# Optimization experiments

Measured on AMD Instinct MI355X. Metric: run time of the kernel, lower is better.

## Reference

```python
import jax, jax.numpy as jnp
import numpy as np

# dims: dim=1024, head_dim=64 (fla default) -> 16 heads; lora dims per TMix.__init__
B, T, D = 8, 2048, 1024
H, HD = 16, 64
DECAY_LR, A_LR, V_LR, G_LR = 64, 64, 32, 160
CHUNK = 64  # chunked scan, mirrors 'chunk' mode state passing
LOG_W_SCALE = -0.6065306597126334  # -exp(-0.5), fla rwkv7 decay soft clamp
GN_EPS = HD * 1e-5  # fla: GroupNorm eps = head_dim * norm_eps


def setup_inputs() -> dict:
    key = jax.random.key(0)
    ks = jax.random.split(key, 22)
    rn = lambda k, shape, s=1.0: jax.random.normal(k, shape, jnp.float32) * s
    s_d = 1.0 / np.sqrt(D).astype(np.float32)
    return dict(
        x=rn(ks[0], (B, T, D)),
        v_first=rn(ks[1], (B, T, D)),
        x_x=rn(ks[2], (6, D), 0.1),           # token-shift mix coefficients (r,w,k,v,a,g)
        W_r=rn(ks[3], (D, D), s_d), W_k=rn(ks[4], (D, D), s_d),
        W_v=rn(ks[5], (D, D), s_d), W_o=rn(ks[6], (D, D), s_d),
        w1=rn(ks[7], (D, DECAY_LR), s_d), w2=rn(ks[8], (DECAY_LR, D), 1.0 / np.sqrt(DECAY_LR)), w0=rn(ks[9], (D,), 0.5),
        a1=rn(ks[10], (D, A_LR), s_d), a2=rn(ks[11], (A_LR, D), 1.0 / np.sqrt(A_LR)), a0=rn(ks[12], (D,), 0.5),
        v1=rn(ks[13], (D, V_LR), s_d), v2=rn(ks[14], (V_LR, D), 1.0 / np.sqrt(V_LR)), v0=rn(ks[15], (D,), 0.5),
        g1=rn(ks[16], (D, G_LR), s_d), g2=rn(ks[17], (G_LR, D), 1.0 / np.sqrt(G_LR)),
        k_k=rn(ks[18], (D,), 0.5), k_a=rn(ks[19], (D,), 0.5), r_k=rn(ks[20], (H, HD), 0.5),
        gn_w=jnp.ones((D,), jnp.float32), gn_b=jnp.zeros((D,), jnp.float32),
    )


def _rwkv7_core(r, logw, k, v, a, b):
    # all [B,T,H,HD]; generalized delta rule: S_t = S_{t-1}*exp(w_t) + (S_{t-1} a_t) b_t^T + v_t k_t^T; o_t = S_t r_t
    nC = T // CHUNK
    to_chunks = lambda z: z.reshape(B, nC, CHUNK, H, HD).transpose(1, 2, 0, 3, 4)  # [nC,C,B,H,HD]
    xs = tuple(map(to_chunks, (r, logw, k, v, a, b)))
    state0 = jnp.zeros((B, H, HD, HD), jnp.float32)  # [B,H,V,K]

    @jax.checkpoint
    def chunk_fn(state, xc):
        def step(s, xt):
            r_t, w_t, k_t, v_t, a_t, b_t = xt  # [B,H,HD] each
            sa = jnp.einsum('bhik,bhk->bhi', s, a_t)
            s = (s * jnp.exp(w_t)[:, :, None, :]
                 + sa[..., None] * b_t[:, :, None, :]
                 + v_t[..., None] * k_t[:, :, None, :])
            return s, jnp.einsum('bhik,bhk->bhi', s, r_t)
        return jax.lax.scan(step, state, xc)

    _, o = jax.lax.scan(chunk_fn, state0, xs)  # o: [nC,C,B,H,HD]
    return o.transpose(2, 0, 1, 3, 4).reshape(B, T, H, HD)


def _forward(x, v_first, x_x, W_r, W_k, W_v, W_o, w1, w2, w0, a1, a2, a0,
             v1, v2, v0, g1, g2, k_k, k_a, r_k, gn_w, gn_b):
    shifted = jnp.pad(x, ((0, 0), (1, 0), (0, 0)))[:, :-1]  # token shift
    delta = shifted - x
    xr, xw, xk, xv, xa, xg = (x + delta * x_x[i] for i in range(6))
    r = xr @ W_r
    logw = LOG_W_SCALE * jax.nn.sigmoid(w0 + jnp.tanh(xw @ w1) @ w2)  # log decay in (-0.6065, 0)
    k = xk @ W_k
    v = xv @ W_v
    # layer_idx != 0: lerp toward first layer's value
    v = v + (v_first - v) * jax.nn.sigmoid(v0 + (xv @ v1) @ v2)
    a = jax.nn.sigmoid(a0 + (xa @ a1) @ a2)  # in-context lr
    g = jax.nn.sigmoid(xg @ g1) @ g2          # output gate
    kk = (k * k_k).reshape(B, T, H, HD)
    kk = kk / jnp.maximum(jnp.linalg.norm(kk, axis=-1, keepdims=True), 1e-12)  # F.normalize
    k = k * (1.0 + (a - 1.0) * k_a)
    heads = lambda z: z.reshape(B, T, H, HD)
    r_h, k_h, v_h, a_h, w_h = heads(r), heads(k), heads(v), heads(a), heads(logw)
    o = _rwkv7_core(r_h, w_h, k_h, v_h, -kk, kk * a_h)
    # GroupNorm over each head (biased variance, torch semantics)
    mu = o.mean(-1, keepdims=True)
    var = o.var(-1, keepdims=True)
    o_n = (o - mu) * jax.lax.rsqrt(var + GN_EPS)
    o_n = o_n * gn_w.reshape(H, HD) + gn_b.reshape(H, HD)
    # rank-1 bonus term
    o_n = o_n + (r_h * k_h * r_k).sum(-1, keepdims=True) * v_h
    out = (o_n.reshape(B, T, D) * g) @ W_o
    return out


def reference(x, v_first, x_x, W_r, W_k, W_v, W_o, w1, w2, w0, a1, a2, a0,
              v1, v2, v0, g1, g2, k_k, k_a, r_k, gn_w, gn_b):
    out = _forward(x, v_first, x_x, W_r, W_k, W_v, W_o, w1, w2, w0, a1, a2, a0,
                   v1, v2, v0, g1, g2, k_k, k_a, r_k, gn_w, gn_b)
    # TMix returns (x_attn, v_first, kv); layer_idx!=0 passes v_first through, kv=None here
    return out, v_first
```

## Files before the change

### kernel.cpp

```cpp
#include <hip/hip_runtime.h>
#include <stdint.h>

#define B_  8
#define T_  2048
#define D_  1024
#define H_  16
#define M_  (B_*T_)
#define LOG_W_SCALE (-0.6065306597126334f)
#define GN_EPS (64.0e-5f)

typedef short short8 __attribute__((ext_vector_type(8)));
typedef float f32x4_t __attribute__((ext_vector_type(4)));

static __device__ __forceinline__ short f2bf(float f) {
  uint32_t u = __builtin_bit_cast(uint32_t, f);
  u += 0x7fffu + ((u >> 16) & 1u);
  return (short)(u >> 16);
}
static __device__ __forceinline__ float bf2f(ushort u) {
  uint32_t x = ((uint32_t)u) << 16;
  return __builtin_bit_cast(float, x);
}
static __device__ __forceinline__ float sigmf_(float x) { return 1.0f / (1.0f + expf(-x)); }

#define OFF_WrT    0ULL
#define OFF_WkT    2097152ULL
#define OFF_WvT    4194304ULL
#define OFF_WoT    6291456ULL
#define OFF_w1T    8388608ULL
#define OFF_a1T    8519680ULL
#define OFF_v1T    8650752ULL
#define OFF_g1T    8716288ULL
#define OFF_w2T    9043968ULL
#define OFF_a2T    9175040ULL
#define OFF_v2T    9306112ULL
#define OFF_g2T    9371648ULL
#define OFF_RB     16777216ULL
#define OFF_KB     50331648ULL
#define OFF_VB     83886080ULL
#define OFF_A2O    117440512ULL
#define OFF_V2O    150994944ULL
#define OFF_GIO    184549376ULL
#define OFF_D1B    218103808ULL
#define OFF_A1B    220200960ULL
#define OFF_V1B    222298112ULL
#define OFF_G1B    223346688ULL
#define WS_NEED    228589568ULL

struct TransDesc { const float* src; ushort* dst; int K, N, blk0, ntn; };
struct TransPack { TransDesc d[12]; };

__global__ __launch_bounds__(256) void trans_kernel(TransPack p) {
  __shared__ float tile[32][33];
  int bid = blockIdx.x;
  int mi = 0;
  #pragma unroll
  for (int i = 1; i < 12; i++) if (bid >= p.d[i].blk0) mi = i;
  TransDesc d = p.d[mi];
  int lb = bid - d.blk0;
  int tn = lb % d.ntn, tk = lb / d.ntn;
  int tx = threadIdx.x & 31, ty = threadIdx.x >> 5;
  #pragma unroll
  for (int i = 0; i < 4; i++) {
    int k = tk*32 + ty + i*8, n = tn*32 + tx;
    float v = (k < d.K && n < d.N) ? d.src[(size_t)k*d.N + n] : 0.f;
    tile[ty + i*8][tx] = v;
  }
  __syncthreads();
  #pragma unroll
  for (int i = 0; i < 4; i++) {
    int n = tn*32 + ty + i*8, k = tk*32 + tx;
    if (n < d.N && k < d.K) d.dst[(size_t)n*d.K + k] = (ushort)f2bf(tile[tx][ty + i*8]);
  }
}

template<bool AMIX, int OMODE>
__global__ __launch_bounds__(256) void gemm_kernel(
    const float* __restrict__ X, const float* __restrict__ xxc,
    const ushort* __restrict__ Abf,
    const ushort* __restrict__ Bt,
    void* __restrict__ Cout, int N, int K)
{
  __shared__ ushort As[128*64];
  __shared__ ushort Bs[128*64];
  int tid = threadIdx.x;
  int bm = blockIdx.y, bn = blockIdx.x;
  int wave = tid >> 6, lane = tid & 63;
  int wr = wave >> 1, wc = wave & 1;
  f32x4_t acc[4][4];
  #pragma unroll
  for (int i = 0; i < 4; i++)
    #pragma unroll
    for (int j = 0; j < 4; j++) acc[i][j] = (f32x4_t){0.f,0.f,0.f,0.f};

  int srow = tid >> 1;
  int scol = (tid & 1) * 32;
  int grow = bm*128 + srow;
  int gbn  = bn*128 + srow;

  for (int k0 = 0; k0 < K; k0 += 64) {
    if constexpr (AMIX) {
      const float* xr = X + (size_t)grow*1024 + k0 + scol;
      bool sh = (grow & (T_-1)) != 0;
      const float* xs = sh ? (xr - 1024) : xr;
      float msk = sh ? 1.f : 0.f;
      const float* cf = xxc + k0 + scol;
      #pragma unroll
      for (int i = 0; i < 4; i++) {
        float4 xa = *(const float4*)(xr + i*8);
        float4 xb = *(const float4*)(xr + i*8 + 4);
        float4 s4 = *(const float4*)(xs + i*8);
        float4 s5 = *(const float4*)(xs + i*8 + 4);
        float4 ca = *(const float4*)(cf + i*8);
        float4 cb = *(const float4*)(cf + i*8 + 4);
        short8 w;
        w[0]=f2bf(xa.x + (s4.x*msk - xa.x)*ca.x);
        w[1]=f2bf(xa.y + (s4.y*msk - xa.y)*ca.y);
        w[2]=f2bf(xa.z + (s4.z*msk - xa.z)*ca.z);
        w[3]=f2bf(xa.w + (s4.w*msk - xa.w)*ca.w);
        w[4]=f2bf(xb.x + (s5.x*msk - xb.x)*cb.x);
        w[5]=f2bf(xb.y + (s5.y*msk - xb.y)*cb.y);
        w[6]=f2bf(xb.z + (s5.z*msk - xb.z)*cb.z);
        w[7]=f2bf(xb.w + (s5.w*msk - xb.w)*cb.w);
        *(short8*)&As[srow*64 + scol + i*8] = w;
      }
    } else {
      const ushort* ap = Abf + (size_t)grow*K + k0 + scol;
      #pragma unroll
      for (int i = 0; i < 4; i++) {
        uint4 u = make_uint4(0,0,0,0);
        if (k0 + scol + i*8 + 8 <= K) u = *(const uint4*)(ap + i*8);
        *(uint4*)&As[srow*64 + scol + i*8] = u;
      }
    }
    {
      const ushort* bp = Bt + (size_t)gbn*K + k0 + scol;
      #pragma unroll
      for (int i = 0; i < 4; i++) {
        uint4 u = make_uint4(0,0,0,0);
        if (gbn < N && (k0 + scol + i*8 + 8 <= K)) u = *(const uint4*)(bp + i*8);
        *(uint4*)&Bs[srow*64 + scol + i*8] = u;
      }
    }
    __syncthreads();
    int l15 = lane & 15, kof = (lane >> 4) * 8;
    #pragma unroll
    for (int ks = 0; ks < 2; ks++) {
      short8 af[4], bfv[4];
      #pragma unroll
      for (int f = 0; f < 4; f++)
        af[f] = *(const short8*)&As[(wr*64 + f*16 + l15)*64 + ks*32 + kof];
      #pragma unroll
      for (int f = 0; f < 4; f++)
        bfv[f] = *(const short8*)&Bs[(wc*64 + f*16 + l15)*64 + ks*32 + kof];
      #pragma unroll
      for (int fr = 0; fr < 4; fr++)
        #pragma unroll
        for (int fc = 0; fc < 4; fc++)
          acc[fr][fc] = __builtin_amdgcn_mfma_f32_16x16x32_bf16(af[fr], bfv[fc], acc[fr][fc], 0, 0, 0);
    }
    __syncthreads();
  }
  int l15 = lane & 15, rg = lane >> 4;
  #pragma unroll
  for (int fr = 0; fr < 4; fr++)
    #pragma unroll
    for (int fc = 0; fc < 4; fc++) {
      int col = bn*128 + wc*64 + fc*16 + l15;
      if (col < N) {
        #pragma unroll
        for (int j = 0; j < 4; j++) {
          int row = bm*128 + wr*64 + fr*16 + rg*4 + j;
          float v = acc[fr][fc][j];
          if constexpr (OMODE == 2) v = tanhf(v);
          if constexpr (OMODE == 3) v = sigmf_(v);
          if constexpr (OMODE == 0) ((float*)Cout)[(size_t)row*N + col] = v;
          else ((ushort*)Cout)[(size_t)row*N + col] = (ushort)f2bf(v);
        }
      }
    }
}

__global__ __launch_bounds__(256, 1) void scan_kernel(
    const ushort* __restrict__ rb, const ushort* __restrict__ kb, const ushort* __restrict__ vb,
    const ushort* __restrict__ d2, const ushort* __restrict__ a2o, const ushort* __restrict__ v2o,
    const float* __restrict__ vfirst,
    const float* __restrict__ w0, const float* __restrict__ a0, const float* __restrict__ v0,
    const float* __restrict__ kkv, const float* __restrict__ kav,
    float* __restrict__ o)
{
  __shared__ float bufs[6][8][64];
  __shared__ float red1[256];
  __shared__ float red2[256];
  int tid = threadIdx.x;
  int bh = blockIdx.x;
  int b = bh >> 4, h = bh & 15;
  int wave = tid >> 6, lane = tid & 63;
  int c0 = wave * 16;
  float S[16];
  #pragma unroll
  for (int i = 0; i < 16; i++) S[i] = 0.f;
  int hc = h*64 + lane;
  float kkc = kkv[hc], kac = kav[hc], w0c = w0[hc], a0c = a0[hc], v0c = v0[hc];

  for (int t0 = 0; t0 < T_; t0 += 8) {
    #pragma unroll
    for (int j = 0; j < 2; j++) {
      int tt = wave + j*4;
      size_t gi = ((size_t)(b*T_ + t0 + tt) * H_ + h) * 64 + lane;
      float kv_ = bf2f(kb[gi]);
      float rv_ = bf2f(rb[gi]);
      float vv_ = bf2f(vb[gi]);
      float dd  = bf2f(d2[gi]);
      float av  = bf2f(a2o[gi]);
      float vo  = bf2f(v2o[gi]);
      float vf  = vfirst[gi];
      float kp = kv_ * kkc;
      float ss = kp * kp;
      ss += __shfl_xor(ss, 1);  ss += __shfl_xor(ss, 2);
      ss += __shfl_xor(ss, 4);  ss += __shfl_xor(ss, 8);
      ss += __shfl_xor(ss, 16); ss += __shfl_xor(ss, 32);
      float inv = 1.0f / fmaxf(sqrtf(ss), 1e-12f);
      float asig = sigmf_(a0c + av);
      float e = expf(LOG_W_SCALE * sigmf_(w0c + dd));
      float kn = kv_ * (1.f + (asig - 1.f) * kac);
      float vl = vv_ + (vf - vv_) * sigmf_(v0c + vo);
      float kkn = kp * inv;
      bufs[0][tt][lane] = rv_;
      bufs[1][tt][lane] = e;
      bufs[2][tt][lane] = kn;
      bufs[3][tt][lane] = vl;
      bufs[4][tt][lane] = -kkn;
      bufs[5][tt][lane] = kkn * asig;
    }
    __syncthreads();
    for (int tt = 0; tt < 8; tt++) {
      const float4* A4 = (const float4*)&bufs[4][tt][c0];
      float p = 0.f;
      #pragma unroll
      for (int j = 0; j < 4; j++) {
        float4 a4 = A4[j];
        p += S[j*4+0]*a4.x + S[j*4+1]*a4.y + S[j*4+2]*a4.z + S[j*4+3]*a4.w;
      }
      red1[wave*64 + lane] = p;
      __syncthreads();
      float sa = red1[lane] + red1[64+lane] + red1[128+lane] + red1[192+lane];
      float vi = bufs[3][tt][lane];
      const float4* E4 = (const float4*)&bufs[1][tt][c0];
      const float4* K4 = (const float4*)&bufs[2][tt][c0];
      const float4* B4 = (const float4*)&bufs[5][tt][c0];
      const float4* R4 = (const float4*)&bufs[0][tt][c0];
      float op = 0.f;
      #pragma unroll
      for (int j = 0; j < 4; j++) {
        float4 e4 = E4[j], k4 = K4[j], b4 = B4[j], r4 = R4[j];
        float s;
        s = S[j*4+0]*e4.x + sa*b4.x + vi*k4.x; S[j*4+0]=s; op += s*r4.x;
        s = S[j*4+1]*e4.y + sa*b4.y + vi*k4.y; S[j*4+1]=s; op += s*r4.y;
        s = S[j*4+2]*e4.z + sa*b4.z + vi*k4.z; S[j*4+2]=s; op += s*r4.z;
        s = S[j*4+3]*e4.w + sa*b4.w + vi*k4.w; S[j*4+3]=s; op += s*r4.w;
      }
      red2[wave*64 + lane] = op;
      __syncthreads();
      if (wave == 0) {
        float oo = red2[lane] + red2[64+lane] + red2[128+lane] + red2[192+lane];
        o[((size_t)(b*T_ + t0 + tt) * H_ + h) * 64 + lane] = oo;
      }
    }
    __syncthreads();
  }
}

__global__ __launch_bounds__(256) void epilogue_kernel(
    const float* __restrict__ o,
    const ushort* __restrict__ rb, const ushort* __restrict__ kb, const ushort* __restrict__ vb,
    const ushort* __restrict__ a2o, const ushort* __restrict__ v2o,
    const float* __restrict__ vfirst,
    ushort* g_io,
    const float* __restrict__ a0, const float* __restrict__ v0, const float* __restrict__ kav,
    const float* __restrict__ rkv,
    const float* __restrict__ gnw, const float* __restrict__ gnb)
{
  int row = blockIdx.x;
  int tid = threadIdx.x;
  int d0 = tid * 4;
  size_t gi = (size_t)row * D_ + d0;
  ushort4 gu = *(const ushort4*)(g_io + gi);
  float4 o4 = *(const float4*)(o + gi);
  ushort4 ru = *(const ushort4*)(rb + gi);
  ushort4 ku = *(const ushort4*)(kb + gi);
  ushort4 vu = *(const ushort4*)(vb + gi);
  ushort4 au = *(const ushort4*)(a2o + gi);
  ushort4 wu = *(const ushort4*)(v2o + gi);
  float4 vf = *(const float4*)(vfirst + gi);
  float4 a04 = *(const float4*)(a0 + d0);
  float4 v04 = *(const float4*)(v0 + d0);
  float4 ka4 = *(const float4*)(kav + d0);
  float4 rk  = *(const float4*)(rkv + d0);
  float4 gw  = *(const float4*)(gnw + d0);
  float4 gb  = *(const float4*)(gnb + d0);

  float s1 = o4.x + o4.y + o4.z + o4.w;
  float s2 = o4.x*o4.x + o4.y*o4.y + o4.z*o4.z + o4.w*o4.w;
  s1 += __shfl_xor(s1, 1, 16); s2 += __shfl_xor(s2, 1, 16);
  s1 += __shfl_xor(s1, 2, 16); s2 += __shfl_xor(s2, 2, 16);
  s1 += __shfl_xor(s1, 4, 16); s2 += __shfl_xor(s2, 4, 16);
  s1 += __shfl_xor(s1, 8, 16); s2 += __shfl_xor(s2, 8, 16);
  float mean = s1 * (1.f/64.f);
  float var  = s2 * (1.f/64.f) - mean*mean;
  float rstd = rsqrtf(var + GN_EPS);

  float r0=bf2f(ru.x), r1=bf2f(ru.y), r2=bf2f(ru.z), r3=bf2f(ru.w);
  float k0=bf2f(ku.x), k1=bf2f(ku.y), k2=bf2f(ku.z), k3=bf2f(ku.w);
  float v0_=bf2f(vu.x), v1_=bf2f(vu.y), v2_=bf2f(vu.z), v3_=bf2f(vu.w);
  float a0_=sigmf_(a04.x+bf2f(au.x)), a1_=sigmf_(a04.y+bf2f(au.y));
  float a2_=sigmf_(a04.z+bf2f(au.z)), a3_=sigmf_(a04.w+bf2f(au.w));
  float kn0=k0*(1.f+(a0_-1.f)*ka4.x), kn1=k1*(1.f+(a1_-1.f)*ka4.y);
  float kn2=k2*(1.f+(a2_-1.f)*ka4.z), kn3=k3*(1.f+(a3_-1.f)*ka4.w);
  float sl;
  sl=sigmf_(v04.x+bf2f(wu.x)); float vl0=v0_+(vf.x-v0_)*sl;
  sl=sigmf_(v04.y+bf2f(wu.y)); float vl1=v1_+(vf.y-v1_)*sl;
  sl=sigmf_(v04.z+bf2f(wu.z)); float vl2=v2_+(vf.z-v2_)*sl;
  sl=sigmf_(v04.w+bf2f(wu.w)); float vl3=v3_+(vf.w-v3_)*sl;

  float bsum = r0*kn0*rk.x + r1*kn1*rk.y + r2*kn2*rk.z + r3*kn3*rk.w;
  bsum += __shfl_xor(bsum, 1, 16); bsum += __shfl_xor(bsum, 2, 16);
  bsum += __shfl_xor(bsum, 4, 16); bsum += __shfl_xor(bsum, 8, 16);

  float g0=bf2f(gu.x), g1=bf2f(gu.y), g2=bf2f(gu.z), g3=bf2f(gu.w);
  float ox = ((o4.x-mean)*rstd*gw.x + gb.x + bsum*vl0) * g0;
  float oy = ((o4.y-mean)*rstd*gw.y + gb.y + bsum*vl1) * g1;
  float oz = ((o4.z-mean)*rstd*gw.z + gb.z + bsum*vl2) * g2;
  float ow = ((o4.w-mean)*rstd*gw.w + gb.w + bsum*vl3) * g3;
  ushort4 u = make_ushort4((ushort)f2bf(ox),(ushort)f2bf(oy),(ushort)f2bf(oz),(ushort)f2bf(ow));
  *((ushort4*)(g_io + gi)) = u;
}

__global__ void marker_kernel(float* p, float v) { p[0] = v; }

extern "C" void kernel_launch(void* const* d_in, const int* in_sizes, int n_in,
                              void* d_out, int out_size, void* d_ws, size_t ws_size,
                              hipStream_t stream) {
  float* dout = (float*)d_out;
  if (ws_size < WS_NEED) {
    hipLaunchKernelGGL(marker_kernel, dim3(1), dim3(1), 0, stream, dout, (float)ws_size);
    return;
  }
  const float* x      = (const float*)d_in[0];
  const float* vfirst = (const float*)d_in[1];
  const float* xx     = (const float*)d_in[2];
  const float* w0v    = (const float*)d_in[9];
  const float* a0v    = (const float*)d_in[12];
  const float* v0v    = (const float*)d_in[15];
  const float* kkv    = (const float*)d_in[18];
  const float* kav    = (const float*)d_in[19];
  const float* rkv    = (const float*)d_in[20];
  const float* gnw    = (const float*)d_in[21];
  const float* gnb    = (const float*)d_in[22];

  char* ws = (char*)d_ws;
  ushort* WrT = (ushort*)(ws + OFF_WrT); ushort* WkT = (ushort*)(ws + OFF_WkT);
  ushort* WvT = (ushort*)(ws + OFF_WvT); ushort* WoT = (ushort*)(ws + OFF_WoT);
  ushort* w1T = (ushort*)(ws + OFF_w1T); ushort* a1T = (ushort*)(ws + OFF_a1T);
  ushort* v1T = (ushort*)(ws + OFF_v1T); ushort* g1T = (ushort*)(ws + OFF_g1T);
  ushort* w2T = (ushort*)(ws + OFF_w2T); ushort* a2T = (ushort*)(ws + OFF_a2T);
  ushort* v2T = (ushort*)(ws + OFF_v2T); ushort* g2T = (ushort*)(ws + OFF_g2T);
  ushort* rb  = (ushort*)(ws + OFF_RB);
  ushort* kb  = (ushort*)(ws + OFF_KB);
  ushort* vb  = (ushort*)(ws + OFF_VB);
  ushort* a2o = (ushort*)(ws + OFF_A2O);
  ushort* v2o = (ushort*)(ws + OFF_V2O);
  ushort* gio = (ushort*)(ws + OFF_GIO);
  ushort* d1b = (ushort*)(ws + OFF_D1B);
  ushort* a1b = (ushort*)(ws + OFF_A1B);
  ushort* v1b = (ushort*)(ws + OFF_V1B);
  ushort* g1b = (ushort*)(ws + OFF_G1B);
  ushort* d2   = (ushort*)dout;
  float*  obuf = dout + 16777216;

  TransPack tp;
  const float* tsrc[12] = {(const float*)d_in[3],(const float*)d_in[4],(const float*)d_in[5],(const float*)d_in[6],
                           (const float*)d_in[7],(const float*)d_in[10],(const float*)d_in[13],(const float*)d_in[16],
                           (const float*)d_in[8],(const float*)d_in[11],(const float*)d_in[14],(const float*)d_in[17]};
  ushort* tdst[12] = {WrT,WkT,WvT,WoT,w1T,a1T,v1T,g1T,w2T,a2T,v2T,g2T};
  int tK[12] = {1024,1024,1024,1024,1024,1024,1024,1024,64,64,32,160};
  int tN[12] = {1024,1024,1024,1024,64,64,32,160,1024,1024,1024,1024};
  int cum = 0;
  for (int i = 0; i < 12; i++) {
    tp.d[i].src = tsrc[i]; tp.d[i].dst = tdst[i];
    tp.d[i].K = tK[i]; tp.d[i].N = tN[i];
    tp.d[i].blk0 = cum; tp.d[i].ntn = (tN[i]+31)/32;
    cum += ((tK[i]+31)/32) * ((tN[i]+31)/32);
  }
  hipLaunchKernelGGL(trans_kernel, dim3(cum), dim3(256), 0, stream, tp);

  #define GEMM_MIX(OM, coef, Bt, C, N) \
    hipLaunchKernelGGL((gemm_kernel<true, OM>), dim3(((N)+127)/128, M_/128), dim3(256), 0, stream, \
                       x, coef, (const ushort*)nullptr, Bt, (void*)(C), N, 1024)
  #define GEMM_PLAIN(OM, A, Bt, C, N, K) \
    hipLaunchKernelGGL((gemm_kernel<false, OM>), dim3(((N)+127)/128, M_/128), dim3(256), 0, stream, \
                       (const float*)nullptr, (const float*)nullptr, A, Bt, (void*)(C), N, K)

  GEMM_MIX(1, xx + 0*1024, WrT, rb, 1024);
  GEMM_MIX(1, xx + 2*1024, WkT, kb, 1024);
  GEMM_MIX(1, xx + 3*1024, WvT, vb, 1024);
  GEMM_MIX(2, xx + 1*1024, w1T, d1b, 64);
  GEMM_MIX(1, xx + 4*1024, a1T, a1b, 64);
  GEMM_MIX(1, xx + 3*1024, v1T, v1b, 32);
  GEMM_MIX(3, xx + 5*1024, g1T, g1b, 160);

  GEMM_PLAIN(1, d1b, w2T, d2,  1024, 64);
  GEMM_PLAIN(1, a1b, a2T, a2o, 1024, 64);
  GEMM_PLAIN(1, v1b, v2T, v2o, 1024, 32);
  GEMM_PLAIN(1, g1b, g2T, gio, 1024, 160);

  hipLaunchKernelGGL(scan_kernel, dim3(B_*H_), dim3(256), 0, stream,
                     rb, kb, vb, d2, a2o, v2o, vfirst, w0v, a0v, v0v, kkv, kav, obuf);

  hipLaunchKernelGGL(epilogue_kernel, dim3(M_), dim3(256), 0, stream,
                     obuf, rb, kb, vb, a2o, v2o, vfirst, gio, a0v, v0v, kav, rkv, gnw, gnb);

  GEMM_PLAIN(0, gio, WoT, dout, 1024, 1024);

  hipMemcpyAsync(dout + 16777216, d_in[1], (size_t)16777216*4, hipMemcpyDeviceToDevice, stream);
}
```

Measured before the change: 3.287 ms.

## Split scan state rows across four blocks per head with shuffle reductions

The recurrent scan now splits the 64 value rows of each head's state across four independent blocks, giving 512 blocks instead of 128, and each wave owns four full state rows with lanes indexing the key dimension. Dot products are reduced with wave-wide xor shuffles instead of shared-memory cross-wave reductions, which removes the two per-timestep __syncthreads. Timesteps are staged in chunks of 16, so there is one barrier per chunk. In exchange, each block recomputes the per-token preprocessing (normalisation, sigmoids, exp) for the whole head, four times redundantly, and each timestep costs many more shuffle instructions.

```diff
diff --git a/kernel.cpp b/kernel.cpp
--- a/kernel.cpp
+++ b/kernel.cpp
@@ -181,7 +181,8 @@
     }
 }
 
-__global__ __launch_bounds__(256, 1) void scan_kernel(
+#define CH 16
+__global__ __launch_bounds__(256, 2) void scan_kernel(
     const ushort* __restrict__ rb, const ushort* __restrict__ kb, const ushort* __restrict__ vb,
     const ushort* __restrict__ d2, const ushort* __restrict__ a2o, const ushort* __restrict__ v2o,
     const float* __restrict__ vfirst,
@@ -189,25 +190,24 @@
     const float* __restrict__ kkv, const float* __restrict__ kav,
     float* __restrict__ o)
 {
-  __shared__ float bufs[6][8][64];
-  __shared__ float red1[256];
-  __shared__ float red2[256];
+  __shared__ float st[6][CH][64];
+  __shared__ float so[CH][64];
   int tid = threadIdx.x;
-  int bh = blockIdx.x;
+  int bid = blockIdx.x;
+  int bh = bid >> 2, q = bid & 3;
   int b = bh >> 4, h = bh & 15;
   int wave = tid >> 6, lane = tid & 63;
-  int c0 = wave * 16;
-  float S[16];
-  #pragma unroll
-  for (int i = 0; i < 16; i++) S[i] = 0.f;
+  int rbase = q*16 + wave*4;
+  float S0 = 0.f, S1 = 0.f, S2 = 0.f, S3 = 0.f;
   int hc = h*64 + lane;
   float kkc = kkv[hc], kac = kav[hc], w0c = w0[hc], a0c = a0[hc], v0c = v0[hc];
-
-  for (int t0 = 0; t0 < T_; t0 += 8) {
+  size_t bhbase = (size_t)b*T_*1024 + h*64;
+
+  for (int t0 = 0; t0 < T_; t0 += CH) {
     #pragma unroll
-    for (int j = 0; j < 2; j++) {
+    for (int j = 0; j < 4; j++) {
       int tt = wave + j*4;
-      size_t gi = ((size_t)(b*T_ + t0 + tt) * H_ + h) * 64 + lane;
+      size_t gi = bhbase + (size_t)(t0+tt)*1024 + lane;
       float kv_ = bf2f(kb[gi]);
       float rv_ = bf2f(rb[gi]);
       float vv_ = bf2f(vb[gi]);
@@ -226,48 +226,44 @@
       float kn = kv_ * (1.f + (asig - 1.f) * kac);
       float vl = vv_ + (vf - vv_) * sigmf_(v0c + vo);
       float kkn = kp * inv;
-      bufs[0][tt][lane] = rv_;
-      bufs[1][tt][lane] = e;
-      bufs[2][tt][lane] = kn;
-      bufs[3][tt][lane] = vl;
-      bufs[4][tt][lane] = -kkn;
-      bufs[5][tt][lane] = kkn * asig;
+      st[0][tt][lane] = rv_;
+      st[1][tt][lane] = e;
+      st[2][tt][lane] = kn;
+      st[3][tt][lane] = vl;
+      st[4][tt][lane] = -kkn;
+      st[5][tt][lane] = kkn * asig;
     }
     __syncthreads();
-    for (int tt = 0; tt < 8; tt++) {
-      const float4* A4 = (const float4*)&bufs[4][tt][c0];
-      float p = 0.f;
-      #pragma unroll
-      for (int j = 0; j < 4; j++) {
-        float4 a4 = A4[j];
-        p += S[j*4+0]*a4.x + S[j*4+1]*a4.y + S[j*4+2]*a4.z + S[j*4+3]*a4.w;
-      }
-      red1[wave*64 + lane] = p;
-      __syncthreads();
-      float sa = red1[lane] + red1[64+lane] + red1[128+lane] + red1[192+lane];
-      float vi = bufs[3][tt][lane];
-      const float4* E4 = (const float4*)&bufs[1][tt][c0];
-      const float4* K4 = (const float4*)&bufs[2][tt][c0];
-      const float4* B4 = (const float4*)&bufs[5][tt][c0];
-      const float4* R4 = (const float4*)&bufs[0][tt][c0];
-      float op = 0.f;
-      #pragma unroll
-      for (int j = 0; j < 4; j++) {
-        float4 e4 = E4[j], k4 = K4[j], b4 = B4[j], r4 = R4[j];
-        float s;
-        s = S[j*4+0]*e4.x + sa*b4.x + vi*k4.x; S[j*4+0]=s; op += s*r4.x;
-        s = S[j*4+1]*e4.y + sa*b4.y + vi*k4.y; S[j*4+1]=s; op += s*r4.y;
-        s = S[j*4+2]*e4.z + sa*b4.z + vi*k4.z; S[j*4+2]=s; op += s*r4.z;
-        s = S[j*4+3]*e4.w + sa*b4.w + vi*k4.w; S[j*4+3]=s; op += s*r4.w;
-      }
-      red2[wave*64 + lane] = op;
-      __syncthreads();
-      if (wave == 0) {
-        float oo = red2[lane] + red2[64+lane] + red2[128+lane] + red2[192+lane];
-        o[((size_t)(b*T_ + t0 + tt) * H_ + h) * 64 + lane] = oo;
-      }
+    for (int tt = 0; tt < CH; ++tt) {
+      float a_l = st[4][tt][lane];
+      float p0 = S0*a_l, p1 = S1*a_l, p2 = S2*a_l, p3 = S3*a_l;
+      #pragma unroll
+      for (int m = 1; m < 64; m <<= 1) {
+        p0 += __shfl_xor(p0, m);
+        p1 += __shfl_xor(p1, m);
+        p2 += __shfl_xor(p2, m);
+        p3 += __shfl_xor(p3, m);
+      }
+      float e_l = st[1][tt][lane], b_l = st[5][tt][lane];
+      float k_l = st[2][tt][lane], r_l = st[0][tt][lane];
+      float4 vv = *(const float4*)&st[3][tt][rbase];
+      S0 = S0*e_l + p0*b_l + vv.x*k_l;
+      S1 = S1*e_l + p1*b_l + vv.y*k_l;
+      S2 = S2*e_l + p2*b_l + vv.z*k_l;
+      S3 = S3*e_l + p3*b_l + vv.w*k_l;
+      float q0 = S0*r_l, q1 = S1*r_l, q2 = S2*r_l, q3 = S3*r_l;
+      #pragma unroll
+      for (int m = 1; m < 64; m <<= 1) {
+        q0 += __shfl_xor(q0, m);
+        q1 += __shfl_xor(q1, m);
+        q2 += __shfl_xor(q2, m);
+        q3 += __shfl_xor(q3, m);
+      }
+      if (lane == 0) *(float4*)&so[tt][rbase] = make_float4(q0, q1, q2, q3);
     }
     __syncthreads();
+    { int tt = tid >> 4, ii = tid & 15;
+      o[bhbase + (size_t)(t0+tt)*1024 + q*16 + ii] = so[tt][q*16 + ii]; }
   }
 }
 
@@ -414,7 +410,7 @@
   GEMM_PLAIN(1, v1b, v2T, v2o, 1024, 32);
   GEMM_PLAIN(1, g1b, g2T, gio, 1024, 160);
 
-  hipLaunchKernelGGL(scan_kernel, dim3(B_*H_), dim3(256), 0, stream,
+  hipLaunchKernelGGL(scan_kernel, dim3(512), dim3(256), 0, stream,
                      rb, kb, vb, d2, a2o, v2o, vfirst, w0v, a0v, v0v, kkv, kav, obuf);
 
   hipLaunchKernelGGL(epilogue_kernel, dim3(M_), dim3(256), 0, stream,
```

Result: slower. 3.929 ms (+19.5%).
